# Kernel tuning notes

Measured on AMD Instinct MI355X. Metric: run time of the kernel, lower is better.

## Reference

```python
import jax, jax.numpy as jnp
import numpy as np

B, C, H, W = 16, 96, 96, 96
K, N, R, CR = 4, 8, 6, 12  # scan dirs, d_state, dt_rank, SE hidden


def channel_ln(x, g, b, eps=1e-6):
    # LayerNorm over channel dim (channel_first)
    mu = jnp.mean(x, axis=1, keepdims=True)
    var = jnp.var(x, axis=1, keepdims=True)
    return (x - mu) * jax.lax.rsqrt(var + eps) * g[None, :, None, None] + b[None, :, None, None]


def conv1x1(x, w, b):
    return jnp.einsum('bchw,dc->bdhw', x, w) + b[None, :, None, None]


def ss2d(x, xproj_w, dtproj_w, dtproj_b, A_logs, Ds, g, bta):
    # 4-direction selective scan (VMamba SS2D core). x: (B,C,H,W)
    Bq, Cq, Hq, Wq = x.shape
    L = Hq * Wq
    xf = x.reshape(Bq, Cq, L)
    xt = jnp.transpose(x, (0, 1, 3, 2)).reshape(Bq, Cq, L)
    xs = jnp.stack([xf, xt, xf[..., ::-1], xt[..., ::-1]], axis=1)  # (B,K,C,L)
    x_dbl = jnp.einsum('bkcl,kdc->bkdl', xs, xproj_w)  # (B,K,R+2N,L)
    dts, Bs, Cs = jnp.split(x_dbl, [R, R + N], axis=2)
    delta = jax.nn.softplus(jnp.einsum('bkrl,kcr->bkcl', dts, dtproj_w) + dtproj_b[None, :, :, None])
    A = -jnp.exp(A_logs)  # (K,C,N)
    u_t = jnp.moveaxis(xs, -1, 0)   # (L,B,K,C)
    d_t = jnp.moveaxis(delta, -1, 0)
    B_t = jnp.moveaxis(Bs, -1, 0)   # (L,B,K,N)
    C_t = jnp.moveaxis(Cs, -1, 0)
    h0 = jnp.zeros((Bq, K, Cq, N), x.dtype)

    @jax.checkpoint
    def step(h, inp):
        u, d, Bv, Cv = inp
        dA = jnp.exp(d[..., None] * A)                      # (B,K,C,N)
        h = dA * h + (d * u)[..., None] * Bv[:, :, None, :]
        return h, jnp.sum(h * Cv[:, :, None, :], axis=-1)   # (B,K,C)

    _, ys = jax.lax.scan(step, h0, (u_t, d_t, B_t, C_t))
    ys = jnp.moveaxis(ys, 0, -1) + Ds[None, :, :, None] * xs  # (B,K,C,L)

    def untrans(yk):
        return jnp.transpose(yk.reshape(Bq, Cq, Wq, Hq), (0, 1, 3, 2)).reshape(Bq, Cq, L)

    out = ys[:, 0] + untrans(ys[:, 1]) + ys[:, 2, :, ::-1] + untrans(ys[:, 3][..., ::-1])
    return channel_ln(out.reshape(Bq, Cq, Hq, Wq), g, bta)


def block_forward(x, ln_g, ln_b, p1_w, p1_b, p2in_w, p2in_b, dw_w, dw_b,
                  xproj_w, dtproj_w, dtproj_b, A_logs, Ds, ssln_g, ssln_b,
                  p2n_g, p2n_b, ca_w1, ca_b1, ca_w2, ca_b2, block_idx):
    h = channel_ln(x, ln_g, ln_b)
    a = jax.nn.silu(conv1x1(h, p1_w, p1_b))
    z = conv1x1(h, p2in_w, p2in_b)
    z = jax.lax.conv_general_dilated(z, dw_w, (1, 1), 'SAME',
                                     dimension_numbers=('NCHW', 'OIHW', 'NCHW'),
                                     feature_group_count=z.shape[1]) + dw_b[None, :, None, None]
    z = jax.nn.silu(z)
    if block_idx % 2 == 0:
        z = jnp.transpose(z, (0, 1, 3, 2))
    else:
        z = z[:, :, ::-1, ::-1]
    z = ss2d(z, xproj_w, dtproj_w, dtproj_b, A_logs, Ds, ssln_g, ssln_b)
    if block_idx % 2 == 0:
        z = jnp.transpose(z, (0, 1, 3, 2))
    else:
        z = z[:, :, ::-1, ::-1]
    z = channel_ln(z, p2n_g, p2n_b)
    y = a * z
    # channel attention (SE)
    s = jnp.mean(y, axis=(2, 3))  # (B,C)
    att = jax.nn.sigmoid(jnp.einsum('cr,br->bc', ca_w2,
                                    jax.nn.silu(jnp.einsum('rc,bc->br', ca_w1, s) + ca_b1)) + ca_b2)
    return x + y * att[:, :, None, None]


def local_mamba(x, params, block_idx):
    b, c, h, w = x.shape
    h2, w2 = h // 2, w // 2
    qs = jnp.stack([x[:, :, :h2, :w2], x[:, :, :h2, w2:],
                    x[:, :, h2:, :w2], x[:, :, h2:, w2:]])  # (4,B,C,h2,w2)
    fn = lambda q, *p: block_forward(q, *p, block_idx)
    outs = jax.vmap(fn)(qs, *params)
    top = jnp.concatenate([outs[0], outs[1]], axis=3)
    bot = jnp.concatenate([outs[2], outs[3]], axis=3)
    return jnp.concatenate([top, bot], axis=2)


def setup_inputs() -> dict:
    key = jax.random.key(0)
    ks = jax.random.split(key, 12)
    rn = lambda k, shape, s=1.0: jax.random.normal(k, shape, jnp.float32) * s
    return dict(
        x=rn(ks[0], (B, C, H, W)),
        ln_g=jnp.ones((4, C)), ln_b=jnp.zeros((4, C)),
        p1_w=rn(ks[1], (4, C, C), C ** -0.5), p1_b=jnp.zeros((4, C)),
        p2in_w=rn(ks[2], (4, C, C), C ** -0.5), p2in_b=jnp.zeros((4, C)),
        dw_w=rn(ks[3], (4, C, 1, 3, 3), 1.0 / 3.0), dw_b=jnp.zeros((4, C)),
        xproj_w=rn(ks[4], (4, K, R + 2 * N, C), C ** -0.5),
        dtproj_w=rn(ks[5], (4, K, C, R), R ** -0.5),
        dtproj_b=rn(ks[6], (4, K, C), 0.1),
        A_logs=jax.random.uniform(ks[7], (4, K, C, N), jnp.float32, 0.0, 1.0),
        Ds=jnp.ones((4, K, C)),
        ssln_g=jnp.ones((4, C)), ssln_b=jnp.zeros((4, C)),
        p2n_g=jnp.ones((4, C)), p2n_b=jnp.zeros((4, C)),
        ca_w1=rn(ks[8], (4, CR, C), C ** -0.5), ca_b1=jnp.zeros((4, CR)),
        ca_w2=rn(ks[9], (4, C, CR), CR ** -0.5), ca_b2=jnp.zeros((4, C)),
        block_idx=0,
    )


def reference(x, ln_g, ln_b, p1_w, p1_b, p2in_w, p2in_b, dw_w, dw_b,
              xproj_w, dtproj_w, dtproj_b, A_logs, Ds, ssln_g, ssln_b,
              p2n_g, p2n_b, ca_w1, ca_b1, ca_w2, ca_b2, block_idx):
    params = (ln_g, ln_b, p1_w, p1_b, p2in_w, p2in_b, dw_w, dw_b,
              xproj_w, dtproj_w, dtproj_b, A_logs, Ds, ssln_g, ssln_b,
              p2n_g, p2n_b, ca_w1, ca_b1, ca_w2, ca_b2)
    return local_mamba(x, params, block_idx)
```

## Files before the change

kernel.cpp:

```cpp
#include <hip/hip_runtime.h>
#include <hip/hip_bf16.h>

#define BQ 16
#define CN 96
#define HQ 48
#define LL 2304
#define NK 4
#define RR 6
#define NNS 8
#define DPJ 22
#define CRr 12
#define LOG2E 1.4426950408889634f

using bf16 = __hip_bfloat16;

__device__ __forceinline__ float b2f(bf16 v) { return __bfloat162float(v); }
__device__ __forceinline__ bf16  f2b(float v){ return __float2bfloat16(v); }
__device__ __forceinline__ float bflo(unsigned u){ return __uint_as_float(u << 16); }
__device__ __forceinline__ float bfhi(unsigned u){ return __uint_as_float(u & 0xffff0000u); }
__device__ __forceinline__ float sigf(float x){ return 1.f / (1.f + __expf(-x)); }
__device__ __forceinline__ float siluf(float x){ return x / (1.f + __expf(-x)); }
__device__ __forceinline__ unsigned packbf(float a, float b){
    unsigned lo = (unsigned)__builtin_bit_cast(unsigned short, f2b(a));
    unsigned hi = (unsigned)__builtin_bit_cast(unsigned short, f2b(b));
    return lo | (hi << 16);
}
__device__ __forceinline__ unsigned rot16(unsigned u){ return (u >> 16) | (u << 16); }
__device__ __forceinline__ void unpack8(uint4 v, float* f){
    f[0]=bflo(v.x); f[1]=bfhi(v.x); f[2]=bflo(v.y); f[3]=bfhi(v.y);
    f[4]=bflo(v.z); f[5]=bfhi(v.z); f[6]=bflo(v.w); f[7]=bfhi(v.w);
}
__device__ __forceinline__ void unpack4(uint2 v, float* f){
    f[0]=bflo(v.x); f[1]=bfhi(v.x); f[2]=bflo(v.y); f[3]=bfhi(v.y);
}
__device__ __forceinline__ float fexp2(float x){
#if __has_builtin(__builtin_amdgcn_exp2f)
    return __builtin_amdgcn_exp2f(x);
#else
    return __expf(x * 0.6931471805599453f);
#endif
}
__device__ __forceinline__ float qxor(float v, int ctrl_b1){
    int x;
    if (ctrl_b1) x = __builtin_amdgcn_mov_dpp(__float_as_int(v), 0xB1, 0xF, 0xF, true);
    else         x = __builtin_amdgcn_mov_dpp(__float_as_int(v), 0x4E, 0xF, 0xF, true);
    return __int_as_float(x);
}

__global__ __launch_bounds__(192) void k_lnconv(
    const float* __restrict__ x, const float* __restrict__ ln_g, const float* __restrict__ ln_b,
    const float* __restrict__ p1w, const float* __restrict__ p1b,
    const float* __restrict__ p2w, const float* __restrict__ p2b,
    bf16* __restrict__ a_out, bf16* __restrict__ z0_out)
{
    const int hh2 = blockIdx.x;
    const int b = blockIdx.y, q = blockIdx.z;
    const int h0 = (q >> 1) * HQ, w0 = (q & 1) * HQ;
    const int tid = threadIdx.x;
    const int qb = q * BQ + b;

    __shared__ alignas(16) bf16 hn[CN * 96];
    __shared__ alignas(16) bf16 wl[CN * 200];
    __shared__ float mu[96], rs[96];

    for (int t = tid; t < CN * CN; t += 192) {
        int d = t / CN, c = t % CN;
        wl[c * 200 + d]      = f2b(p1w[(q * CN + d) * CN + c]);
        wl[c * 200 + 96 + d] = f2b(p2w[(q * CN + d) * CN + c]);
    }
    for (int t = tid; t < CN * 24; t += 192) {
        int c = t / 24, v = t % 24;
        int row = v / 12, col = (v % 12) * 4;
        float4 xv = *reinterpret_cast<const float4*>(
            &x[((b * CN + c) * 96 + h0 + 2 * hh2 + row) * 96 + w0 + col]);
        uint2 pk; pk.x = packbf(xv.x, xv.y); pk.y = packbf(xv.z, xv.w);
        *reinterpret_cast<uint2*>(&hn[c * 96 + v * 4]) = pk;
    }
    __syncthreads();
    if (tid < 96) {
        float s = 0.f, s2 = 0.f;
        for (int c = 0; c < CN; ++c) { float v = b2f(hn[c * 96 + tid]); s += v; s2 += v * v; }
        float m = s * (1.f / 96.f);
        float var = s2 * (1.f / 96.f) - m * m;
        mu[tid] = m; rs[tid] = rsqrtf(var + 1e-6f);
    }
    __syncthreads();
    for (int t = tid; t < CN * 96; t += 192) {
        int c = t / 96, p = t % 96;
        float g = ln_g[q * CN + c], bb = ln_b[q * CN + c];
        hn[t] = f2b((b2f(hn[t]) - mu[p]) * rs[p] * g + bb);
    }
    __syncthreads();
    const int rg = tid >> 3, pg = tid & 7;
    const int row0 = rg * 8, pp0 = pg * 12;
    float acc[8][12];
    #pragma unroll
    for (int i = 0; i < 8; ++i)
        #pragma unroll
        for (int j = 0; j < 12; ++j) acc[i][j] = 0.f;

    for (int c = 0; c < CN; ++c) {
        uint4 wv = *reinterpret_cast<const uint4*>(&wl[c * 200 + row0]);
        float w[8];
        w[0] = bflo(wv.x); w[1] = bfhi(wv.x);
        w[2] = bflo(wv.y); w[3] = bfhi(wv.y);
        w[4] = bflo(wv.z); w[5] = bfhi(wv.z);
        w[6] = bflo(wv.w); w[7] = bfhi(wv.w);
        uint2 ha = *reinterpret_cast<const uint2*>(&hn[c * 96 + pp0]);
        uint2 hb = *reinterpret_cast<const uint2*>(&hn[c * 96 + pp0 + 4]);
        uint2 hc = *reinterpret_cast<const uint2*>(&hn[c * 96 + pp0 + 8]);
        float hv[12];
        hv[0] = bflo(ha.x); hv[1] = bfhi(ha.x); hv[2]  = bflo(ha.y); hv[3]  = bfhi(ha.y);
        hv[4] = bflo(hb.x); hv[5] = bfhi(hb.x); hv[6]  = bflo(hb.y); hv[7]  = bfhi(hb.y);
        hv[8] = bflo(hc.x); hv[9] = bfhi(hc.x); hv[10] = bflo(hc.y); hv[11] = bfhi(hc.y);
        #pragma unroll
        for (int i = 0; i < 8; ++i)
            #pragma unroll
            for (int j = 0; j < 12; ++j)
                acc[i][j] = fmaf(w[i], hv[j], acc[i][j]);
    }
    const int lbase = (2 * hh2 + pp0 / 48) * 48 + (pp0 % 48);
    #pragma unroll
    for (int i = 0; i < 8; ++i) {
        int row = row0 + i;
        bool isA = row < 96;
        int d = isA ? row : row - 96;
        float bias = isA ? p1b[q * CN + d] : p2b[q * CN + d];
        int oidx = (qb * CN + d) * LL + lbase;
        float v[12];
        #pragma unroll
        for (int j = 0; j < 12; ++j) v[j] = acc[i][j] + bias;
        if (isA) {
            #pragma unroll
            for (int j = 0; j < 12; ++j) v[j] = siluf(v[j]);
        }
        uint2 w0p, w1p, w2p;
        w0p.x = packbf(v[0], v[1]);  w0p.y = packbf(v[2], v[3]);
        w1p.x = packbf(v[4], v[5]);  w1p.y = packbf(v[6], v[7]);
        w2p.x = packbf(v[8], v[9]);  w2p.y = packbf(v[10], v[11]);
        bf16* dst = isA ? a_out : z0_out;
        *reinterpret_cast<uint2*>(&dst[oidx])     = w0p;
        *reinterpret_cast<uint2*>(&dst[oidx + 4]) = w1p;
        *reinterpret_cast<uint2*>(&dst[oidx + 8]) = w2p;
    }
}

__global__ __launch_bounds__(256) void k_dwconv(
    const bf16* __restrict__ z0, const float* __restrict__ dww, const float* __restrict__ dwb,
    const int* __restrict__ bidx, bf16* __restrict__ zt, bf16* __restrict__ ztT)
{
    const int c = blockIdx.x, b = blockIdx.y, q = blockIdx.z;
    const int tid = threadIdx.x;
    const int base = ((q * BQ + b) * CN + c) * LL;
    __shared__ float zin[LL];
    __shared__ float zo[48 * 49];
    for (int t = tid; t < 288; t += 256) {
        uint4 v = *reinterpret_cast<const uint4*>(&z0[base + t * 8]);
        float f[8]; unpack8(v, f);
        *reinterpret_cast<float4*>(&zin[t * 8])     = make_float4(f[0], f[1], f[2], f[3]);
        *reinterpret_cast<float4*>(&zin[t * 8 + 4]) = make_float4(f[4], f[5], f[6], f[7]);
    }
    float wk[9];
    #pragma unroll
    for (int i = 0; i < 9; ++i) wk[i] = dww[(q * CN + c) * 9 + i];
    const float bias = dwb[q * CN + c];
    __syncthreads();
    for (int t = tid; t < LL; t += 256) {
        int hh = t / 48, ww = t % 48;
        float s = bias;
        #pragma unroll
        for (int dy = -1; dy <= 1; ++dy)
            #pragma unroll
            for (int dx = -1; dx <= 1; ++dx) {
                int yy = hh + dy, xx = ww + dx;
                if (yy >= 0 && yy < 48 && xx >= 0 && xx < 48)
                    s = fmaf(wk[(dy + 1) * 3 + (dx + 1)], zin[yy * 48 + xx], s);
            }
        zo[hh * 49 + ww] = siluf(s);
    }
    __syncthreads();
    const bool even = ((bidx[0] & 1) == 0);
    for (int t = tid; t < LL; t += 256) {
        int i = t / 48, j = t % 48;
        float vz, vzT;
        if (even) { vz = zo[j * 49 + i];               vzT = zo[i * 49 + j]; }
        else      { vz = zo[(47 - i) * 49 + (47 - j)]; vzT = zo[(47 - j) * 49 + (47 - i)]; }
        zt[base + t]  = f2b(vz);
        ztT[base + t] = f2b(vzT);
    }
}

__global__ __launch_bounds__(256) void k_xdbl(
    const bf16* __restrict__ zt, const bf16* __restrict__ ztT,
    const float* __restrict__ xprojw, bf16* __restrict__ xdbl)
{
    const int lt = blockIdx.x, k = blockIdx.y, qb = blockIdx.z;
    const int tid = threadIdx.x;
    const int l0 = lt * 192;
    const int q = qb >> 4;
    __shared__ alignas(16) bf16 ul[CN * 200];
    __shared__ alignas(16) bf16 wl[CN * 24];
    const bf16* __restrict__ src = (k & 1) ? ztT : zt;
    const bool rev = (k >= 2);
    for (int t = tid; t < CN * 24; t += 256) {
        int cc = t / 24, j0 = (t % 24) * 8;
        uint4 v;
        if (!rev) {
            v = *reinterpret_cast<const uint4*>(&src[(size_t)(qb * CN + cc) * LL + l0 + j0]);
        } else {
            v = *reinterpret_cast<const uint4*>(&src[(size_t)(qb * CN + cc) * LL + (LL - (l0 + j0) - 8)]);
            uint4 r; r.x = rot16(v.w); r.y = rot16(v.z); r.z = rot16(v.y); r.w = rot16(v.x);
            v = r;
        }
        *reinterpret_cast<uint4*>(&ul[cc * 200 + j0]) = v;
    }
    for (int t = tid; t < DPJ * CN; t += 256) {
        int d = t / CN, c = t % CN;
        wl[c * 24 + d] = f2b(xprojw[(q * NK + k) * DPJ * CN + t]);
    }
    __syncthreads();
    if (tid < 176) {
        const int dp = tid / 16, lg = tid % 16;
        const int d0 = dp * 2, llp = lg * 12;
        float acc0[12], acc1[12];
        #pragma unroll
        for (int j = 0; j < 12; ++j) { acc0[j] = 0.f; acc1[j] = 0.f; }
        for (int c = 0; c < CN; ++c) {
            unsigned wv = *reinterpret_cast<const unsigned*>(&wl[c * 24 + d0]);
            float w0 = bflo(wv), w1 = bfhi(wv);
            uint2 ua = *reinterpret_cast<const uint2*>(&ul[c * 200 + llp]);
            uint2 ub = *reinterpret_cast<const uint2*>(&ul[c * 200 + llp + 4]);
            uint2 uc = *reinterpret_cast<const uint2*>(&ul[c * 200 + llp + 8]);
            float uf[12];
            unpack4(ua, uf); unpack4(ub, uf + 4); unpack4(uc, uf + 8);
            #pragma unroll
            for (int j = 0; j < 12; ++j) {
                acc0[j] = fmaf(w0, uf[j], acc0[j]);
                acc1[j] = fmaf(w1, uf[j], acc1[j]);
            }
        }
        int ob = (qb * NK + k) * DPJ * LL + l0 + llp;
        uint2 o0a, o0b, o0c, o1a, o1b, o1c;
        o0a.x = packbf(acc0[0], acc0[1]);  o0a.y = packbf(acc0[2], acc0[3]);
        o0b.x = packbf(acc0[4], acc0[5]);  o0b.y = packbf(acc0[6], acc0[7]);
        o0c.x = packbf(acc0[8], acc0[9]);  o0c.y = packbf(acc0[10], acc0[11]);
        o1a.x = packbf(acc1[0], acc1[1]);  o1a.y = packbf(acc1[2], acc1[3]);
        o1b.x = packbf(acc1[4], acc1[5]);  o1b.y = packbf(acc1[6], acc1[7]);
        o1c.x = packbf(acc1[8], acc1[9]);  o1c.y = packbf(acc1[10], acc1[11]);
        *reinterpret_cast<uint2*>(&xdbl[ob + d0 * LL])           = o0a;
        *reinterpret_cast<uint2*>(&xdbl[ob + d0 * LL + 4])       = o0b;
        *reinterpret_cast<uint2*>(&xdbl[ob + d0 * LL + 8])       = o0c;
        *reinterpret_cast<uint2*>(&xdbl[ob + (d0 + 1) * LL])     = o1a;
        *reinterpret_cast<uint2*>(&xdbl[ob + (d0 + 1) * LL + 4]) = o1b;
        *reinterpret_cast<uint2*>(&xdbl[ob + (d0 + 1) * LL + 8]) = o1c;
    }
}


#define SCAN_BARRIER() asm volatile("s_waitcnt lgkmcnt(0)\n\ts_barrier" ::: "memory")

#define UWORD(NUA, IDX) (((IDX) & 3) == 0 ? NUA[(IDX) >> 2].x : \
                         ((IDX) & 3) == 1 ? NUA[(IDX) >> 2].y : \
                         ((IDX) & 3) == 2 ? NUA[(IDX) >> 2].z : NUA[(IDX) >> 2].w)

__global__ __launch_bounds__(192) void k_scan(
    const bf16* __restrict__ zt, const bf16* __restrict__ ztT,
    const bf16* __restrict__ xdbl,
    const float* __restrict__ dtw_g, const float* __restrict__ dtb_g,
    const float* __restrict__ Alog_g, const float* __restrict__ Ds_g,
    bf16* __restrict__ ys)
{
    const int bid = blockIdx.x;
    const int ch2 = bid & 1, k = (bid >> 1) & 3, qb = bid >> 3, q = qb >> 4;
    const int qk = q * NK + k;
    const int tid = threadIdx.x;
    const int ca = tid >> 2, p = tid & 3;
    const int c = ch2 * 48 + ca;

    __shared__ float dd3[3][48 * 52];
    __shared__ float xr3[3][6 * 52];
    __shared__ float bcv3[3][48 * 16];

    const float* wp = dtw_g + (size_t)qk * CN * RR + c * RR;
    float wdt[6];
    {
        float2 wa = *reinterpret_cast<const float2*>(wp);
        float2 wb = *reinterpret_cast<const float2*>(wp + 2);
        float2 wc = *reinterpret_cast<const float2*>(wp + 4);
        wdt[0] = wa.x; wdt[1] = wa.y; wdt[2] = wb.x; wdt[3] = wb.y; wdt[4] = wc.x; wdt[5] = wc.y;
    }
    const float dtbc = dtb_g[qk * CN + c];
    const float A0L = -__expf(Alog_g[((size_t)qk * CN + c) * NNS + 2 * p])     * LOG2E;
    const float A1L = -__expf(Alog_g[((size_t)qk * CN + c) * NNS + 2 * p + 1]) * LOG2E;
    const float Dc = Ds_g[qk * CN + c];
    float h0 = 0.f, h1 = 0.f;

    const bf16* __restrict__ src = (k & 1) ? ztT : zt;
    const bool rev = (k >= 2);
    const int ja = p * 12;

    const bf16* gu = src + (size_t)(qb * CN + c) * LL + (rev ? (LL - 48) : 0);
    const int ustep = rev ? -48 : 48;

    const bool xload = (tid < 132);
    const int vr = tid / 6, jx = (tid % 6) * 8;
    const bf16* gx = xdbl + (size_t)(qb * NK + k) * (DPJ * LL) + (size_t)vr * LL + jx;
    int bccol = 0;
    if (vr >= 6) {
        int v = vr - 6;
        int n = v & 7;
        bccol = (n >> 1) * 4 + ((v >= 8) ? 2 : 0) + (n & 1);
    }

    bf16* yp = ys + (size_t)(qb * NK + k) * (CN * LL) + (size_t)c * LL;

    uint4 px0 = {0,0,0,0};
    if (xload) px0 = *reinterpret_cast<const uint4*>(gx);
    uint4 u_a[6], u_b[6];
    #pragma unroll
    for (int i = 0; i < 6; ++i) u_a[i] = *reinterpret_cast<const uint4*>(gu + i * 8);
    gu += ustep;
    #pragma unroll
    for (int i = 0; i < 6; ++i) u_b[i] = *reinterpret_cast<const uint4*>(gu + i * 8);
    gu += ustep;
    uint4 px_a = {0,0,0,0}, px_b = {0,0,0,0};
    if (xload) {
        px_a = *reinterpret_cast<const uint4*>(gx + 48);
        px_b = *reinterpret_cast<const uint4*>(gx + 96);
        gx += 144;
    }

    #define COMMIT_BLOCK(PXV, XRB, BCB) do {                                          \
        if (xload) {                                                                  \
            float g[8]; unpack8(PXV, g);                                              \
            if (vr < 6) {                                                             \
                *reinterpret_cast<float4*>(&(XRB)[vr * 52 + jx])                      \
                    = make_float4(g[0], g[1], g[2], g[3]);                            \
                *reinterpret_cast<float4*>(&(XRB)[vr * 52 + jx + 4])                  \
                    = make_float4(g[4], g[5], g[6], g[7]);                            \
            } else {                                                                  \
                _Pragma("unroll")                                                     \
                for (int i = 0; i < 8; ++i) (BCB)[(jx + i) * 16 + bccol] = g[i];      \
            }                                                                         \
        }                                                                             \
    } while (0)

    #define DELTA_BLOCK(XRB, DDB) do {                                                \
        float acc[12];                                                                \
        _Pragma("unroll")                                                             \
        for (int i = 0; i < 12; ++i) acc[i] = dtbc;                                   \
        _Pragma("unroll")                                                             \
        for (int r = 0; r < 6; ++r) {                                                 \
            float4 d0 = *reinterpret_cast<const float4*>(&(XRB)[r * 52 + ja]);        \
            float4 d1 = *reinterpret_cast<const float4*>(&(XRB)[r * 52 + ja + 4]);    \
            float4 d2 = *reinterpret_cast<const float4*>(&(XRB)[r * 52 + ja + 8]);    \
            float wr_ = wdt[r];                                                       \
            acc[0] = fmaf(wr_, d0.x, acc[0]);  acc[1] = fmaf(wr_, d0.y, acc[1]);      \
            acc[2] = fmaf(wr_, d0.z, acc[2]);  acc[3] = fmaf(wr_, d0.w, acc[3]);      \
            acc[4] = fmaf(wr_, d1.x, acc[4]);  acc[5] = fmaf(wr_, d1.y, acc[5]);      \
            acc[6] = fmaf(wr_, d1.z, acc[6]);  acc[7] = fmaf(wr_, d1.w, acc[7]);      \
            acc[8] = fmaf(wr_, d2.x, acc[8]);  acc[9] = fmaf(wr_, d2.y, acc[9]);      \
            acc[10] = fmaf(wr_, d2.z, acc[10]); acc[11] = fmaf(wr_, d2.w, acc[11]);   \
        }                                                                             \
        _Pragma("unroll")                                                             \
        for (int i = 0; i < 12; ++i) {                                                \
            float a = acc[i];                                                         \
            acc[i] = (a > 15.f) ? a : __logf(1.f + __expf(a));                        \
        }                                                                             \
        float4* dp = reinterpret_cast<float4*>(&(DDB)[ca * 52 + ja]);                 \
        dp[0] = make_float4(acc[0], acc[1], acc[2], acc[3]);                          \
        dp[1] = make_float4(acc[4], acc[5], acc[6], acc[7]);                          \
        dp[2] = make_float4(acc[8], acc[9], acc[10], acc[11]);                        \
    } while (0)

    COMMIT_BLOCK(px0, xr3[0], bcv3[0]);
    SCAN_BARRIER();
    DELTA_BLOCK(xr3[0], dd3[0]);

    int b_cur = 0, b_nxt = 1, b_thd = 2;

    #define SCAN_BODY(CH, UC, PX) do {                                                \
        const int ch_ = (CH);                                                         \
                     \
        uint4 nu[6];                                                                  \
        if (!rev) {                                                                   \
            nu[0] = UC[0]; nu[1] = UC[1]; nu[2] = UC[2];                              \
            nu[3] = UC[3]; nu[4] = UC[4]; nu[5] = UC[5];                              \
        } else {                                                                      \
            _Pragma("unroll")                                                         \
            for (int qq = 0; qq < 6; ++qq) {                                          \
                nu[qq].x = rot16(UC[5 - qq].w); nu[qq].y = rot16(UC[5 - qq].z);       \
                nu[qq].z = rot16(UC[5 - qq].y); nu[qq].w = rot16(UC[5 - qq].x);       \
            }                                                                         \
        }                                                                             \
                                          \
        if (ch_ < 47) COMMIT_BLOCK(PX, xr3[b_nxt], bcv3[b_nxt]);                      \
                      \
        if (ch_ < 45 && xload) { PX = *reinterpret_cast<const uint4*>(gx); gx += 48; }\
                                      \
        SCAN_BARRIER();                                                               \
                          \
        if (ch_ < 47) DELTA_BLOCK(xr3[b_nxt], dd3[b_nxt]);                            \
                                                                \
        {                                                                             \
            const int l0 = ch_ * 48;                                                  \
            const float* ddc = &dd3[b_cur][ca * 52];                                  \
            const float* bcc = &bcv3[b_cur][p * 4];                                   \
            _Pragma("unroll")                                                         \
            for (int gg = 0; gg < 6; ++gg) {                                          \
                unsigned pk[4];                                                       \
                _Pragma("unroll")                                                     \
                for (int half = 0; half < 2; ++half) {                                \
                    const int j0 = gg * 8 + half * 4;                                 \
                    float4 d4 = *reinterpret_cast<const float4*>(ddc + j0);           \
                    const float* df = reinterpret_cast<const float*>(&d4);            \
                    _Pragma("unroll")                                                 \
                    for (int s = 0; s < 4; ++s) {                                     \
                        const int j = j0 + s;                                         \
                        const unsigned uwv = UWORD(nu, j >> 1);                       \
                        float u = (j & 1) ? bfhi(uwv) : bflo(uwv);                    \
                        float d = df[s];                                              \
                        float4 bq = *reinterpret_cast<const float4*>(bcc + j * 16);   \
                        float du = d * u;                                             \
                        float dA0 = fexp2(d * A0L);                                   \
                        float dA1 = fexp2(d * A1L);                                   \
                        h0 = fmaf(dA0, h0, du * bq.x);                                \
                        h1 = fmaf(dA1, h1, du * bq.y);                                \
                        float y = fmaf(h0, bq.z, h1 * bq.w);                          \
                        y += qxor(y, 1); y += qxor(y, 0);                             \
                        y = fmaf(Dc, u, y);                                           \
                        unsigned hb = (unsigned)__builtin_bit_cast(unsigned short, f2b(y)); \
                        const int sl = half * 4 + s;                                  \
                        if (sl & 1) pk[sl >> 1] |= hb << 16; else pk[sl >> 1] = hb;   \
                    }                                                                 \
                }                                                                     \
                if (p == 0) {                                                         \
                    uint4 wv4; wv4.x = pk[0]; wv4.y = pk[1]; wv4.z = pk[2]; wv4.w = pk[3]; \
                    *reinterpret_cast<uint4*>(yp + l0 + gg * 8) = wv4;                \
                }                                                                     \
            }                                                                         \
        }                                                                             \
                    \
        if (ch_ < 46) {                                                               \
            _Pragma("unroll")                                                         \
            for (int i = 0; i < 6; ++i) UC[i] = *reinterpret_cast<const uint4*>(gu + i * 8); \
            gu += ustep;                                                              \
        }                                                                             \
                                                               \
        { int tb = b_cur; b_cur = b_nxt; b_nxt = b_thd; b_thd = tb; }                 \
    } while (0)

    for (int t = 0; t < 24; ++t) {
        SCAN_BODY(2 * t,     u_a, px_a);
        SCAN_BODY(2 * t + 1, u_b, px_b);
    }

    #undef SCAN_BODY
    #undef DELTA_BLOCK
    #undef COMMIT_BLOCK
}

__global__ __launch_bounds__(256) void k_sum(
    const bf16* __restrict__ ys, bf16* __restrict__ s_out)
{
    const int c = blockIdx.x, b = blockIdx.y, q = blockIdx.z;
    const int qb = q * BQ + b;
    const int tid = threadIdx.x;
    __shared__ float t0[48 * 49];
    __shared__ float t2[48 * 49];
    const size_t base0 = ((size_t)(qb * NK + 0) * CN + c) * LL;
    const size_t base1 = ((size_t)(qb * NK + 1) * CN + c) * LL;
    const size_t base2 = ((size_t)(qb * NK + 2) * CN + c) * LL;
    const size_t base3 = ((size_t)(qb * NK + 3) * CN + c) * LL;
    for (int idx = tid; idx < 288; idx += 256) {
        int e0 = idx * 8, h = e0 / 48, w = e0 % 48;
        float f[8];
        unpack8(*reinterpret_cast<const uint4*>(&ys[base0 + e0]), f);
        #pragma unroll
        for (int i = 0; i < 8; ++i) t0[h * 49 + w + i] = f[i];
        unpack8(*reinterpret_cast<const uint4*>(&ys[base2 + e0]), f);
        #pragma unroll
        for (int i = 0; i < 8; ++i) t2[h * 49 + w + i] = f[i];
    }
    __syncthreads();
    const size_t cbase = ((size_t)qb * CN + c) * LL;
    for (int idx = tid; idx < 288; idx += 256) {
        int m0 = idx * 8, ww = m0 / 48, hh = m0 % 48;
        float f1[8], f3[8];
        unpack8(*reinterpret_cast<const uint4*>(&ys[base1 + m0]), f1);
        unpack8(*reinterpret_cast<const uint4*>(&ys[base3 + (LL - 8 - m0)]), f3);
        float o[8];
        #pragma unroll
        for (int i = 0; i < 8; ++i) {
            float v0 = t0[(hh + i) * 49 + ww];
            float v2 = t2[(47 - hh - i) * 49 + (47 - ww)];
            o[i] = v0 + f1[i] + v2 + f3[7 - i];
        }
        uint4 w;
        w.x = packbf(o[0], o[1]); w.y = packbf(o[2], o[3]);
        w.z = packbf(o[4], o[5]); w.w = packbf(o[6], o[7]);
        *reinterpret_cast<uint4*>(&s_out[cbase + m0]) = w;
    }
}

__global__ __launch_bounds__(256) void k_combine(
    const bf16* __restrict__ s_in, const bf16* __restrict__ a_in,
    const float* __restrict__ ssg, const float* __restrict__ ssb,
    const float* __restrict__ png, const float* __restrict__ pnb,
    const int* __restrict__ bidx,
    bf16* __restrict__ y_out, float* __restrict__ s_buf)
{
    const int ww = blockIdx.x, b = blockIdx.y, q = blockIdx.z;
    const int qb = q * BQ + b;
    const int tid = threadIdx.x;
    __shared__ float o[CN * 48];
    __shared__ float mu[48], rs[48];
    for (int v = tid; v < 576; v += 256) {
        int e0 = v * 8, cc = e0 / 48, hh = e0 % 48;
        float f[8];
        unpack8(*reinterpret_cast<const uint4*>(&s_in[((size_t)qb * CN + cc) * LL + ww * 48 + hh]), f);
        #pragma unroll
        for (int i = 0; i < 8; ++i) o[cc * 48 + hh + i] = f[i];
    }
    __syncthreads();
    if (tid < 48) {
        float s = 0.f, s2 = 0.f;
        for (int cc = 0; cc < CN; ++cc) { float v = o[cc * 48 + tid]; s += v; s2 += v * v; }
        float m = s * (1.f / 96.f), var = s2 * (1.f / 96.f) - m * m;
        mu[tid] = m; rs[tid] = rsqrtf(var + 1e-6f);
    }
    __syncthreads();
    for (int t = tid; t < CN * 48; t += 256) {
        int cc = t / 48, hh = t % 48;
        o[t] = (o[t] - mu[hh]) * rs[hh] * ssg[q * CN + cc] + ssb[q * CN + cc];
    }
    __syncthreads();
    if (tid < 48) {
        float s = 0.f, s2 = 0.f;
        for (int cc = 0; cc < CN; ++cc) { float v = o[cc * 48 + tid]; s += v; s2 += v * v; }
        float m = s * (1.f / 96.f), var = s2 * (1.f / 96.f) - m * m;
        mu[tid] = m; rs[tid] = rsqrtf(var + 1e-6f);
    }
    __syncthreads();
    const bool even = ((bidx[0] & 1) == 0);
    if (even) {
        for (int v = tid; v < 576; v += 256) {
            int e0 = v * 8, cc = e0 / 48, hh = e0 % 48;
            size_t oidx = ((size_t)qb * CN + cc) * LL + ww * 48 + hh;
            float af[8];
            unpack8(*reinterpret_cast<const uint4*>(&a_in[oidx]), af);
            float yv[8];
            #pragma unroll
            for (int i = 0; i < 8; ++i) {
                float z2 = (o[cc * 48 + hh + i] - mu[hh + i]) * rs[hh + i] * png[q * CN + cc] + pnb[q * CN + cc];
                yv[i] = af[i] * z2;
                o[cc * 48 + hh + i] = yv[i];
            }
            uint4 w;
            w.x = packbf(yv[0], yv[1]); w.y = packbf(yv[2], yv[3]);
            w.z = packbf(yv[4], yv[5]); w.w = packbf(yv[6], yv[7]);
            *reinterpret_cast<uint4*>(&y_out[oidx]) = w;
        }
    } else {
        for (int t = tid; t < CN * 48; t += 256) {
            int cc = t / 48, hh = t % 48;
            float z2 = (o[t] - mu[hh]) * rs[hh] * png[q * CN + cc] + pnb[q * CN + cc];
            size_t oidx = ((size_t)qb * CN + cc) * LL + (47 - hh) * 48 + (47 - ww);
            float yv = b2f(a_in[oidx]) * z2;
            y_out[oidx] = f2b(yv);
            o[t] = yv;
        }
    }
    __syncthreads();
    if (tid < CN) {
        float s = 0.f;
        for (int j = 0; j < 48; ++j) s += o[tid * 48 + j];
        atomicAdd(&s_buf[qb * CN + tid], s);
    }
}

__global__ __launch_bounds__(256) void k_final(
    const float* __restrict__ x, const bf16* __restrict__ y_in,
    const float* __restrict__ s_buf,
    const float* __restrict__ w1, const float* __restrict__ b1,
    const float* __restrict__ w2, const float* __restrict__ b2,
    float* __restrict__ out)
{
    const int c = blockIdx.x, b = blockIdx.y, q = blockIdx.z;
    const int h0 = (q >> 1) * HQ, w0 = (q & 1) * HQ;
    const int qb = q * BQ + b;
    const int tid = threadIdx.x;
    __shared__ float tl[CRr];
    __shared__ float attv;
    if (tid < CRr) {
        float acc = b1[q * CRr + tid];
        const float* wr = w1 + (q * CRr + tid) * CN;
        const float* sb = s_buf + qb * CN;
        for (int cc = 0; cc < CN; ++cc)
            acc = fmaf(wr[cc], sb[cc] * (1.f / (float)LL), acc);
        tl[tid] = siluf(acc);
    }
    __syncthreads();
    if (tid == 0) {
        float acc = b2[q * CN + c];
        #pragma unroll
        for (int r = 0; r < CRr; ++r) acc = fmaf(w2[(q * CN + c) * CRr + r], tl[r], acc);
        attv = sigf(acc);
    }
    __syncthreads();
    const float av = attv;
    const size_t ybase = (size_t)(qb * CN + c) * LL;
    const int xb = (b * CN + c) * 9216 + h0 * 96 + w0;
    for (int t = tid; t < LL / 8; t += 256) {
        int e0 = t * 8;
        int gi = xb + (e0 / 48) * 96 + (e0 % 48);
        uint4 yv = *reinterpret_cast<const uint4*>(&y_in[ybase + e0]);
        float yf[8]; unpack8(yv, yf);
        float4 xa = *reinterpret_cast<const float4*>(&x[gi]);
        float4 xc = *reinterpret_cast<const float4*>(&x[gi + 4]);
        float4 o0 = {xa.x + yf[0]*av, xa.y + yf[1]*av, xa.z + yf[2]*av, xa.w + yf[3]*av};
        float4 o1 = {xc.x + yf[4]*av, xc.y + yf[5]*av, xc.z + yf[6]*av, xc.w + yf[7]*av};
        *reinterpret_cast<float4*>(&out[gi])     = o0;
        *reinterpret_cast<float4*>(&out[gi + 4]) = o1;
    }
}

extern "C" void kernel_launch(void* const* d_in, const int* in_sizes, int n_in,
                              void* d_out, int out_size, void* d_ws, size_t ws_size,
                              hipStream_t stream)
{
    (void)in_sizes; (void)n_in; (void)out_size; (void)ws_size;
    const float* x       = (const float*)d_in[0];
    const float* ln_g    = (const float*)d_in[1];
    const float* ln_b    = (const float*)d_in[2];
    const float* p1_w    = (const float*)d_in[3];
    const float* p1_b    = (const float*)d_in[4];
    const float* p2in_w  = (const float*)d_in[5];
    const float* p2in_b  = (const float*)d_in[6];
    const float* dw_w    = (const float*)d_in[7];
    const float* dw_b    = (const float*)d_in[8];
    const float* xproj_w = (const float*)d_in[9];
    const float* dtproj_w= (const float*)d_in[10];
    const float* dtproj_b= (const float*)d_in[11];
    const float* A_logs  = (const float*)d_in[12];
    const float* Ds      = (const float*)d_in[13];
    const float* ssln_g  = (const float*)d_in[14];
    const float* ssln_b  = (const float*)d_in[15];
    const float* p2n_g   = (const float*)d_in[16];
    const float* p2n_b   = (const float*)d_in[17];
    const float* ca_w1   = (const float*)d_in[18];
    const float* ca_b1   = (const float*)d_in[19];
    const float* ca_w2   = (const float*)d_in[20];
    const float* ca_b2   = (const float*)d_in[21];
    const int*  bidx     = (const int*)d_in[22];
    float* out = (float*)d_out;

    char* ws = (char*)d_ws;
    const size_t off_a    = 0;
    const size_t off_zt   = 28311552;
    const size_t off_ztT  = 56623104;
    const size_t off_xdbl = 84934656;
    const size_t off_ys   = 110886912;
    const size_t off_z0   = off_ys;
    const size_t off_s    = off_zt;
    const size_t off_y    = off_ztT;
    const size_t off_sb   = 224133120;

    bf16*  a_buf   = (bf16*)(ws + off_a);
    bf16*  zt_buf  = (bf16*)(ws + off_zt);
    bf16*  ztT_buf = (bf16*)(ws + off_ztT);
    bf16*  xdbl_buf= (bf16*)(ws + off_xdbl);
    bf16*  ys_buf  = (bf16*)(ws + off_ys);
    bf16*  z0_buf  = (bf16*)(ws + off_z0);
    bf16*  s_sum   = (bf16*)(ws + off_s);
    bf16*  y_buf   = (bf16*)(ws + off_y);
    float* s_buf   = (float*)(ws + off_sb);

    (void)hipMemsetAsync(ws + off_sb, 0, 24576, stream);

    k_lnconv<<<dim3(24, 16, 4), 192, 0, stream>>>(
        x, ln_g, ln_b, p1_w, p1_b, p2in_w, p2in_b, a_buf, z0_buf);
    k_dwconv<<<dim3(96, 16, 4), 256, 0, stream>>>(
        z0_buf, dw_w, dw_b, bidx, zt_buf, ztT_buf);
    k_xdbl<<<dim3(12, 4, 64), 256, 0, stream>>>(
        zt_buf, ztT_buf, xproj_w, xdbl_buf);
    k_scan<<<dim3(512), 192, 0, stream>>>(
        zt_buf, ztT_buf, xdbl_buf, dtproj_w, dtproj_b, A_logs, Ds, ys_buf);
    k_sum<<<dim3(96, 16, 4), 256, 0, stream>>>(
        ys_buf, s_sum);
    k_combine<<<dim3(48, 16, 4), 256, 0, stream>>>(
        s_sum, a_buf, ssln_g, ssln_b, p2n_g, p2n_b, bidx, y_buf, s_buf);
    k_final<<<dim3(96, 16, 4), 256, 0, stream>>>(
        x, y_buf, s_buf, ca_w1, ca_b1, ca_w2, ca_b2, out);
}
```

Baseline: 736.8 us.

## Split scan kernel into producer and consumer warps for delta computation

The selective-scan kernel now launches 384 threads per block. The first 192 threads only run the recurrence, and the other 192 act as producers that load x_dbl, stage B/C values and compute the softplus delta for a later chunk, using a three-deep shared-memory ring. This moves delta and dtproj work off the serial scan's critical path so it overlaps with the recurrence. The cost is twice the threads per block, which may lower occupancy, plus an extra barrier per chunk step.

```diff
diff --git a/kernel.cpp b/kernel.cpp
--- a/kernel.cpp
+++ b/kernel.cpp
@@ -263,7 +263,9 @@
                          ((IDX) & 3) == 1 ? NUA[(IDX) >> 2].y : \
                          ((IDX) & 3) == 2 ? NUA[(IDX) >> 2].z : NUA[(IDX) >> 2].w)
 
-__global__ __launch_bounds__(192) void k_scan(
+#define ROT3(v) (v) = ((v) == 2) ? 0 : ((v) + 1)
+
+__global__ __launch_bounds__(384) void k_scan(
     const bf16* __restrict__ zt, const bf16* __restrict__ ztT,
     const bf16* __restrict__ xdbl,
     const float* __restrict__ dtw_g, const float* __restrict__ dtb_g,
@@ -274,36 +276,31 @@
     const int ch2 = bid & 1, k = (bid >> 1) & 3, qb = bid >> 3, q = qb >> 4;
     const int qk = q * NK + k;
     const int tid = threadIdx.x;
-    const int ca = tid >> 2, p = tid & 3;
+    const bool isScan = (tid < 192);
+    const int lt = isScan ? tid : (tid - 192);
+    const int ca = lt >> 2, p = lt & 3;
     const int c = ch2 * 48 + ca;
 
     __shared__ float dd3[3][48 * 52];
     __shared__ float xr3[3][6 * 52];
     __shared__ float bcv3[3][48 * 16];
 
-    const float* wp = dtw_g + (size_t)qk * CN * RR + c * RR;
-    float wdt[6];
-    {
+    const bf16* __restrict__ src = (k & 1) ? ztT : zt;
+    const bool rev = (k >= 2);
+    const int ja = p * 12;
+
+    float wdt[6] = {0.f, 0.f, 0.f, 0.f, 0.f, 0.f};
+    float dtbc = 0.f;
+    if (!isScan) {
+        const float* wp = dtw_g + (size_t)qk * CN * RR + c * RR;
         float2 wa = *reinterpret_cast<const float2*>(wp);
         float2 wb = *reinterpret_cast<const float2*>(wp + 2);
         float2 wc = *reinterpret_cast<const float2*>(wp + 4);
         wdt[0] = wa.x; wdt[1] = wa.y; wdt[2] = wb.x; wdt[3] = wb.y; wdt[4] = wc.x; wdt[5] = wc.y;
-    }
-    const float dtbc = dtb_g[qk * CN + c];
-    const float A0L = -__expf(Alog_g[((size_t)qk * CN + c) * NNS + 2 * p])     * LOG2E;
-    const float A1L = -__expf(Alog_g[((size_t)qk * CN + c) * NNS + 2 * p + 1]) * LOG2E;
-    const float Dc = Ds_g[qk * CN + c];
-    float h0 = 0.f, h1 = 0.f;
-
-    const bf16* __restrict__ src = (k & 1) ? ztT : zt;
-    const bool rev = (k >= 2);
-    const int ja = p * 12;
-
-    const bf16* gu = src + (size_t)(qb * CN + c) * LL + (rev ? (LL - 48) : 0);
-    const int ustep = rev ? -48 : 48;
-
-    const bool xload = (tid < 132);
-    const int vr = tid / 6, jx = (tid % 6) * 8;
+        dtbc = dtb_g[qk * CN + c];
+    }
+    const bool xload = (!isScan) && (lt < 132);
+    const int vr = lt / 6, jx = (lt % 6) * 8;
     const bf16* gx = xdbl + (size_t)(qb * NK + k) * (DPJ * LL) + (size_t)vr * LL + jx;
     int bccol = 0;
     if (vr >= 6) {
@@ -312,23 +309,16 @@
         bccol = (n >> 1) * 4 + ((v >= 8) ? 2 : 0) + (n & 1);
     }
 
+    float A0L = 0.f, A1L = 0.f, Dc = 0.f;
+    if (isScan) {
+        A0L = -__expf(Alog_g[((size_t)qk * CN + c) * NNS + 2 * p])     * LOG2E;
+        A1L = -__expf(Alog_g[((size_t)qk * CN + c) * NNS + 2 * p + 1]) * LOG2E;
+        Dc = Ds_g[qk * CN + c];
+    }
+    float h0 = 0.f, h1 = 0.f;
+    const bf16* gu = src + (size_t)(qb * CN + c) * LL + (rev ? (LL - 48) : 0);
+    const int ustep = rev ? -48 : 48;
     bf16* yp = ys + (size_t)(qb * NK + k) * (CN * LL) + (size_t)c * LL;
-
-    uint4 px0 = {0,0,0,0};
-    if (xload) px0 = *reinterpret_cast<const uint4*>(gx);
-    uint4 u_a[6], u_b[6];
-    #pragma unroll
-    for (int i = 0; i < 6; ++i) u_a[i] = *reinterpret_cast<const uint4*>(gu + i * 8);
-    gu += ustep;
-    #pragma unroll
-    for (int i = 0; i < 6; ++i) u_b[i] = *reinterpret_cast<const uint4*>(gu + i * 8);
-    gu += ustep;
-    uint4 px_a = {0,0,0,0}, px_b = {0,0,0,0};
-    if (xload) {
-        px_a = *reinterpret_cast<const uint4*>(gx + 48);
-        px_b = *reinterpret_cast<const uint4*>(gx + 96);
-        gx += 144;
-    }
 
     #define COMMIT_BLOCK(PXV, XRB, BCB) do {                                          \
         if (xload) {                                                                  \
@@ -373,15 +363,46 @@
         dp[2] = make_float4(acc[8], acc[9], acc[10], acc[11]);                        \
     } while (0)
 
-    COMMIT_BLOCK(px0, xr3[0], bcv3[0]);
+    uint4 u_a[6], u_b[6];
+    uint4 px_a = {0,0,0,0}, px_b = {0,0,0,0}, px1 = {0,0,0,0};
+    if (isScan) {
+        #pragma unroll
+        for (int i = 0; i < 6; ++i) u_a[i] = *reinterpret_cast<const uint4*>(gu + i * 8);
+        gu += ustep;
+        #pragma unroll
+        for (int i = 0; i < 6; ++i) u_b[i] = *reinterpret_cast<const uint4*>(gu + i * 8);
+        gu += ustep;
+    } else {
+        uint4 px0 = {0,0,0,0};
+        if (xload) {
+            px0  = *reinterpret_cast<const uint4*>(gx);
+            px1  = *reinterpret_cast<const uint4*>(gx + 48);
+            px_a = *reinterpret_cast<const uint4*>(gx + 96);
+            px_b = *reinterpret_cast<const uint4*>(gx + 144);
+            gx += 192;
+        }
+        COMMIT_BLOCK(px0, xr3[0], bcv3[0]);
+    }
     SCAN_BARRIER();
-    DELTA_BLOCK(xr3[0], dd3[0]);
-
-    int b_cur = 0, b_nxt = 1, b_thd = 2;
-
-    #define SCAN_BODY(CH, UC, PX) do {                                                \
+    if (!isScan) {
+        DELTA_BLOCK(xr3[0], dd3[0]);
+        COMMIT_BLOCK(px1, xr3[1], bcv3[1]);
+    }
+    SCAN_BARRIER();
+
+    int s_cur = 0;
+    int d_idx = 1, c_idx = 2;
+
+    #define PROD_BODY(CH, PX) do {                                                    \
+        const int chp_ = (CH);                                                        \
+        if (chp_ + 2 < 48) COMMIT_BLOCK(PX, xr3[c_idx], bcv3[c_idx]);                 \
+        if (chp_ + 4 < 48 && xload) { PX = *reinterpret_cast<const uint4*>(gx); gx += 48; } \
+        if (chp_ + 1 < 48) DELTA_BLOCK(xr3[d_idx], dd3[d_idx]);                       \
+        ROT3(d_idx); ROT3(c_idx);                                                     \
+    } while (0)
+
+    #define SCAN_CHUNK(CH, UC) do {                                                   \
         const int ch_ = (CH);                                                         \
-                     \
         uint4 nu[6];                                                                  \
         if (!rev) {                                                                   \
             nu[0] = UC[0]; nu[1] = UC[1]; nu[2] = UC[2];                              \
@@ -393,19 +414,10 @@
                 nu[qq].z = rot16(UC[5 - qq].y); nu[qq].w = rot16(UC[5 - qq].x);       \
             }                                                                         \
         }                                                                             \
-                                          \
-        if (ch_ < 47) COMMIT_BLOCK(PX, xr3[b_nxt], bcv3[b_nxt]);                      \
-                      \
-        if (ch_ < 45 && xload) { PX = *reinterpret_cast<const uint4*>(gx); gx += 48; }\
-                                      \
-        SCAN_BARRIER();                                                               \
-                          \
-        if (ch_ < 47) DELTA_BLOCK(xr3[b_nxt], dd3[b_nxt]);                            \
-                                                                \
         {                                                                             \
             const int l0 = ch_ * 48;                                                  \
-            const float* ddc = &dd3[b_cur][ca * 52];                                  \
-            const float* bcc = &bcv3[b_cur][p * 4];                                   \
+            const float* ddc = &dd3[s_cur][ca * 52];                                  \
+            const float* bcc = &bcv3[s_cur][p * 4];                                   \
             _Pragma("unroll")                                                         \
             for (int gg = 0; gg < 6; ++gg) {                                          \
                 unsigned pk[4];                                                       \
@@ -440,22 +452,25 @@
                 }                                                                     \
             }                                                                         \
         }                                                                             \
-                    \
-        if (ch_ < 46) {                                                               \
+        if (ch_ + 2 < 48) {                                                           \
             _Pragma("unroll")                                                         \
             for (int i = 0; i < 6; ++i) UC[i] = *reinterpret_cast<const uint4*>(gu + i * 8); \
             gu += ustep;                                                              \
         }                                                                             \
-                                                               \
-        { int tb = b_cur; b_cur = b_nxt; b_nxt = b_thd; b_thd = tb; }                 \
+        ROT3(s_cur);                                                                  \
     } while (0)
 
     for (int t = 0; t < 24; ++t) {
-        SCAN_BODY(2 * t,     u_a, px_a);
-        SCAN_BODY(2 * t + 1, u_b, px_b);
-    }
-
-    #undef SCAN_BODY
+        if (isScan) SCAN_CHUNK(2 * t, u_a);
+        else        PROD_BODY(2 * t, px_a);
+        SCAN_BARRIER();
+        if (isScan) SCAN_CHUNK(2 * t + 1, u_b);
+        else        PROD_BODY(2 * t + 1, px_b);
+        SCAN_BARRIER();
+    }
+
+    #undef SCAN_CHUNK
+    #undef PROD_BODY
     #undef DELTA_BLOCK
     #undef COMMIT_BLOCK
 }
@@ -684,7 +699,7 @@
         z0_buf, dw_w, dw_b, bidx, zt_buf, ztT_buf);
     k_xdbl<<<dim3(12, 4, 64), 256, 0, stream>>>(
         zt_buf, ztT_buf, xproj_w, xdbl_buf);
-    k_scan<<<dim3(512), 192, 0, stream>>>(
+    k_scan<<<dim3(512), 384, 0, stream>>>(
         zt_buf, ztT_buf, xdbl_buf, dtproj_w, dtproj_b, A_logs, Ds, ys_buf);
     k_sum<<<dim3(96, 16, 4), 256, 0, stream>>>(
         ys_buf, s_sum);
```

After: 736.8 us. Within noise of the previous version (+0.0%).
